# Kernel optimization log

Measured on AMD Instinct MI355X. Metric: run time of the kernel, lower is better.

Reference implementation:

```python
import jax, jax.numpy as jnp
import numpy as np

L = 6          # number of GNN layers
D = 128        # feature_dim (d_model)
H = 4          # num_heads (hardcoded in AttentionalPropagation)
DH = D // H    # per-head dim
N = 2048       # number of segments/keypoints per frame
B = 1          # batch
NAMES = ["self", "cross"] * (L // 2)
EPS = 1e-5     # InstanceNorm1d eps


def _conv1(W, b, x):
    # Conv1d kernel_size=1: W [out,in], x [b,in,n] -> [b,out,n]
    return jnp.einsum('oi,bin->bon', W, x) + b[None, :, None]


def _inorm(x):
    # InstanceNorm1d (affine=False): normalize over the length axis per (batch, channel)
    m = jnp.mean(x, axis=-1, keepdims=True)
    v = jnp.mean((x - m) ** 2, axis=-1, keepdims=True)
    return (x - m) * jax.lax.rsqrt(v + EPS)


def _attn_block(x, src, p):
    Wq, bq, Wk, bk, Wv, bv, Wm, bm, W1, b1, W2, b2 = p
    b_dim, _, n = x.shape
    # view(b, dim, heads, -1): channel axis split as (DH, H)
    q = _conv1(Wq, bq, x).reshape(b_dim, DH, H, -1)
    k = _conv1(Wk, bk, src).reshape(b_dim, DH, H, -1)
    v = _conv1(Wv, bv, src).reshape(b_dim, DH, H, -1)
    scores = jnp.einsum('bdhn,bdhm->bhnm', q, k) / jnp.sqrt(jnp.asarray(DH, x.dtype))
    prob = jax.nn.softmax(scores, axis=-1)
    msg = jnp.einsum('bhnm,bdhm->bdhn', prob, v).reshape(b_dim, D, -1)
    msg = _conv1(Wm, bm, msg)
    # MLP([2D, 2D, D]): Conv1d -> InstanceNorm1d -> ReLU -> Conv1d
    h = _conv1(W1, b1, jnp.concatenate([x, msg], axis=1))
    h = jax.nn.relu(_inorm(h))
    return _conv1(W2, b2, h)


def setup_inputs() -> dict:
    key = jax.random.key(0)
    ks = jax.random.split(key, 14)
    s = 0.05
    f32 = jnp.float32
    return {
        "desc0": jax.random.normal(ks[0], (B, D, N), f32),
        "desc1": jax.random.normal(ks[1], (B, D, N), f32),
        "Wq": jax.random.normal(ks[2], (L, D, D), f32) * s,
        "bq": jnp.zeros((L, D), f32),
        "Wk": jax.random.normal(ks[3], (L, D, D), f32) * s,
        "bk": jnp.zeros((L, D), f32),
        "Wv": jax.random.normal(ks[4], (L, D, D), f32) * s,
        "bv": jnp.zeros((L, D), f32),
        "Wm": jax.random.normal(ks[5], (L, D, D), f32) * s,
        "bm": jnp.zeros((L, D), f32),
        "W1": jax.random.normal(ks[6], (L, 2 * D, 2 * D), f32) * s,
        "b1": jnp.zeros((L, 2 * D), f32),
        "W2": jax.random.normal(ks[7], (L, D, 2 * D), f32) * s,
        "b2": jnp.zeros((L, D), f32),  # nn.init.constant_(mlp[-1].bias, 0.0)
    }


def reference(desc0, desc1, Wq, bq, Wk, bk, Wv, bv, Wm, bm, W1, b1, W2, b2):
    params = (Wq, bq, Wk, bk, Wv, bv, Wm, bm, W1, b1, W2, b2)
    for l in range(L):
        p = tuple(a[l] for a in params)
        if NAMES[l] == 'cross':
            src0, src1 = desc1, desc0
        else:
            src0, src1 = desc0, desc1
        delta0 = _attn_block(desc0, src0, p)
        delta1 = _attn_block(desc1, src1, p)
        desc0 = desc0 + delta0
        desc1 = desc1 + delta1
    return desc0, desc1
```

## Files before the change

### kernel.cpp

```cpp
#include <hip/hip_runtime.h>

#define NN 2048
#define DDIM 128
#define NHEAD 4
#define DH 32
#define NL 6

typedef __attribute__((ext_vector_type(8))) __bf16 bf16x8;
typedef __attribute__((ext_vector_type(4))) float f32x4;

__device__ __forceinline__ unsigned int f2bf(float x) {
  unsigned int u = __float_as_uint(x);
  u += 0x7fff + ((u >> 16) & 1);
  return u >> 16;
}
__device__ __forceinline__ unsigned int pk2(float a, float b) {
  return f2bf(a) | (f2bf(b) << 16);
}
__device__ __forceinline__ float bf2f(unsigned short u) {
  return __uint_as_float(((unsigned int)u) << 16);
}

__global__ __launch_bounds__(256) void wcast_kernel(
    const float* __restrict__ Wq, const float* __restrict__ Wk,
    const float* __restrict__ Wv, const float* __restrict__ W1,
    const float* __restrict__ W2,
    unsigned short* __restrict__ Wqkv, unsigned short* __restrict__ Wb2,
    unsigned short* __restrict__ Wmix) {
  int idx = (blockIdx.x * 256 + threadIdx.x) * 4;
  if (idx >= 688128) return;
  const float* src; unsigned short* dst; int soff, doff;
  if (idx < 98304)       { src = Wq; soff = idx; dst = Wqkv; doff = idx; }
  else if (idx < 196608) { src = Wk; soff = idx - 98304; dst = Wqkv; doff = idx; }
  else if (idx < 294912) { src = Wv; soff = idx - 196608; dst = Wqkv; doff = idx; }
  else if (idx < 491520) { src = W2; soff = idx - 294912; dst = Wb2; doff = soff; }
  else {
    int f = idx - 491520;
    int l = f >> 15, rem = f & 32767;
    int i = rem >> 7, c = rem & 127;
    src = W1; soff = (l << 16) + (i << 8) + c;
    dst = Wmix; doff = (l << 16) + (i << 8) + c;
  }
  float4 v = *(const float4*)&src[soff];
  uint2 p = { pk2(v.x, v.y), pk2(v.z, v.w) };
  *(uint2*)&dst[doff] = p;
}

__global__ __launch_bounds__(256) void wfuse_kernel(
    const float* __restrict__ W1, const float* __restrict__ Wm,
    unsigned short* __restrict__ Wmix,
    const float* __restrict__ bmv, const float* __restrict__ b1,
    float* __restrict__ b1m) {
  const int l = blockIdx.z;
  const int bj = blockIdx.x * 64;
  const int bi = blockIdx.y * 64;
  __shared__ float Ws[32][65];
  __shared__ float Xs[32][64];
  const int t = threadIdx.x;
  const int ti = (t >> 4) << 2;
  const int tj = (t & 15) << 2;
  float acc[4][4] = {{0.f}};
  for (int k0 = 0; k0 < 128; k0 += 32) {
#pragma unroll
    for (int i = 0; i < 8; ++i) {
      int e = t + i * 256;
      int ii = e >> 5, kk = e & 31;
      Ws[kk][ii] = W1[(size_t)(l << 16) + (bi + ii) * 256 + 128 + k0 + kk];
    }
#pragma unroll
    for (int i = 0; i < 2; ++i) {
      int e = t + i * 256;
      int r = e >> 4, c4 = e & 15;
      *(float4*)&Xs[r][c4 * 4] = *(const float4*)&Wm[(size_t)l * 16384 + (k0 + r) * 128 + bj + c4 * 4];
    }
    __syncthreads();
#pragma unroll
    for (int kk = 0; kk < 32; ++kk) {
      float a[4];
      a[0] = Ws[kk][ti]; a[1] = Ws[kk][ti + 1]; a[2] = Ws[kk][ti + 2]; a[3] = Ws[kk][ti + 3];
      float4 b4 = *(const float4*)&Xs[kk][tj];
      float bb[4] = {b4.x, b4.y, b4.z, b4.w};
#pragma unroll
      for (int i = 0; i < 4; ++i)
#pragma unroll
        for (int j = 0; j < 4; ++j) acc[i][j] += a[i] * bb[j];
    }
    __syncthreads();
  }
#pragma unroll
  for (int i = 0; i < 4; ++i) {
    uint2 p = { pk2(acc[i][0], acc[i][1]), pk2(acc[i][2], acc[i][3]) };
    *(uint2*)&Wmix[(size_t)(l << 16) + (bi + ti + i) * 256 + 128 + bj + tj] = p;
  }
  if (blockIdx.x == 0 && blockIdx.y == 0) {
    float a = b1[l * 256 + t];
    const float* wr = &W1[(size_t)(l << 16) + t * 256 + 128];
    const float* bp = &bmv[l * 128];
    for (int k = 0; k < 128; k += 4)
      a += wr[k] * bp[k] + wr[k + 1] * bp[k + 1] + wr[k + 2] * bp[k + 2] + wr[k + 3] * bp[k + 3];
    b1m[l * 256 + t] = a;
  }
}

__global__ __launch_bounds__(256) void desc_cast_kernel(
    const float* __restrict__ d0, const float* __restrict__ d1,
    unsigned short* __restrict__ t0, unsigned short* __restrict__ t1,
    float* __restrict__ o0, float* __restrict__ o1) {
  const float* D = blockIdx.y ? d1 : d0;
  unsigned short* T = blockIdx.y ? t1 : t0;
  float* O = blockIdx.y ? o1 : o0;
  const int n0 = blockIdx.x * 64;
  const int t = threadIdx.x;
  __shared__ __align__(16) unsigned short L[64 * 136];
#pragma unroll
  for (int i = 0; i < 8; ++i) {
    int idx = t + i * 256;
    int c = idx >> 4, nj = (idx & 15) * 4;
    float4 v = *(const float4*)&D[(size_t)c * NN + n0 + nj];
    *(float4*)&O[(size_t)c * NN + n0 + nj] = v;
    L[(nj + 0) * 136 + c] = (unsigned short)f2bf(v.x);
    L[(nj + 1) * 136 + c] = (unsigned short)f2bf(v.y);
    L[(nj + 2) * 136 + c] = (unsigned short)f2bf(v.z);
    L[(nj + 3) * 136 + c] = (unsigned short)f2bf(v.w);
  }
  __syncthreads();
#pragma unroll
  for (int i = 0; i < 4; ++i) {
    int idx = t + i * 256;
    int n = idx >> 4, cj = (idx & 15) * 8;
    uint4 v = *(const uint4*)&L[n * 136 + cj];
    *(uint4*)&T[(size_t)(n0 + n) * 128 + cj] = v;
  }
}

struct MOp {
  const unsigned short* A;
  const float* bias;
  const unsigned short* B1;
  const unsigned short* B2;
  unsigned short* Cb;
  float* Cf;
  const float* Sp;
  int K, ldb, ldc, mode;
};
struct MOps8 { MOp op[8]; };

__global__ __launch_bounds__(256) void mfma_gemm_kernel(MOps8 P) {
  const MOp g = P.op[blockIdx.z];
  const int t = threadIdx.x;
  const int w = t >> 6, lane = t & 63;
  const int col = lane & 15, Qd = lane >> 4;
  const int bm = blockIdx.y * 64;
  const int bn = blockIdx.x * 128;

  __shared__ __align__(16) unsigned short Ws[64 * 40];
  __shared__ __align__(16) unsigned short Xs[128 * 40];
  __shared__ float meanL[256], rstdL[256];
  __shared__ float swS[4][64], swQ[4][64];

  if (g.mode == 4) {
    float s = g.Sp[t * 2], ss = g.Sp[t * 2 + 1];
    float mean = s * (1.0f / NN);
    float var = fmaxf(ss * (1.0f / NN) - mean * mean, 0.f);
    meanL[t] = mean;
    rstdL[t] = rsqrtf(var + 1e-5f);
  }
  if (g.mode == 0 && g.Cf && blockIdx.x == 0 && blockIdx.y == 0) {
    g.Cf[t] = 0.f;
    g.Cf[t + 256] = 0.f;
  }

  f32x4 acc[4][2];
#pragma unroll
  for (int mt = 0; mt < 4; ++mt)
#pragma unroll
    for (int nt = 0; nt < 2; ++nt) acc[mt][nt] = (f32x4){0.f, 0.f, 0.f, 0.f};

  for (int k0 = 0; k0 < g.K; k0 += 32) {
    __syncthreads();
    {
      int row = t >> 2, ko = (t & 3) * 8;
      *(uint4*)&Ws[row * 40 + ko] =
          *(const uint4*)&g.A[(size_t)(bm + row) * g.K + k0 + ko];
    }
    const unsigned short* Bp = g.B1;
    int kk0 = k0;
    if (g.B2 && k0 >= 128) { Bp = g.B2; kk0 = k0 - 128; }
#pragma unroll
    for (int i = 0; i < 2; ++i) {
      int idx = t + i * 256;
      int row = idx >> 2, ko = (idx & 3) * 8;
      uint4 v = *(const uint4*)&Bp[(size_t)(bn + row) * g.ldb + kk0 + ko];
      if (g.mode == 4) {
        union { uint4 q; unsigned short us[8]; } u;
        u.q = v;
#pragma unroll
        for (int j = 0; j < 8; ++j) {
          int k = k0 + ko + j;
          float x = bf2f(u.us[j]);
          x = fmaxf((x - meanL[k]) * rstdL[k], 0.f);
          u.us[j] = (unsigned short)f2bf(x);
        }
        v = u.q;
      }
      *(uint4*)&Xs[row * 40 + ko] = v;
    }
    __syncthreads();
    bf16x8 af[4], bfr[2];
#pragma unroll
    for (int mt = 0; mt < 4; ++mt)
      af[mt] = *(const bf16x8*)&Ws[(mt * 16 + col) * 40 + Qd * 8];
#pragma unroll
    for (int nt = 0; nt < 2; ++nt)
      bfr[nt] = *(const bf16x8*)&Xs[(w * 32 + nt * 16 + col) * 40 + Qd * 8];
#pragma unroll
    for (int mt = 0; mt < 4; ++mt)
#pragma unroll
      for (int nt = 0; nt < 2; ++nt)
        acc[mt][nt] = __builtin_amdgcn_mfma_f32_16x16x32_bf16(af[mt], bfr[nt], acc[mt][nt], 0, 0, 0);
  }

#pragma unroll
  for (int mt = 0; mt < 4; ++mt) {
    const int c0 = bm + mt * 16 + Qd * 4;
    const float b0 = g.bias[c0], b1 = g.bias[c0 + 1];
    const float b2 = g.bias[c0 + 2], b3 = g.bias[c0 + 3];
    float sA[4] = {0.f, 0.f, 0.f, 0.f}, sQ[4] = {0.f, 0.f, 0.f, 0.f};
#pragma unroll
    for (int nt = 0; nt < 2; ++nt) {
      const int n = bn + w * 32 + nt * 16 + col;
      f32x4 a = acc[mt][nt];
      float v0 = a[0] + b0, v1 = a[1] + b1, v2 = a[2] + b2, v3 = a[3] + b3;
      if (g.mode <= 2) {
        if (g.mode == 0) {
          const float sc = 0.25503488f;
          v0 *= sc; v1 *= sc; v2 *= sc; v3 *= sc;
        }
        const int d = c0 >> 2;
        if (g.mode == 1) {
          g.Cb[((size_t)0 * NN + n) * 32 + d] = (unsigned short)f2bf(v0);
          g.Cb[((size_t)1 * NN + n) * 32 + d] = (unsigned short)f2bf(v1);
          g.Cb[((size_t)2 * NN + n) * 32 + d] = (unsigned short)f2bf(v2);
          g.Cb[((size_t)3 * NN + n) * 32 + d] = (unsigned short)f2bf(v3);
        } else {
          g.Cb[(size_t)(0 * 32 + d) * NN + n] = (unsigned short)f2bf(v0);
          g.Cb[(size_t)(1 * 32 + d) * NN + n] = (unsigned short)f2bf(v1);
          g.Cb[(size_t)(2 * 32 + d) * NN + n] = (unsigned short)f2bf(v2);
          g.Cb[(size_t)(3 * 32 + d) * NN + n] = (unsigned short)f2bf(v3);
        }
      } else if (g.mode == 5) {
        uint2 pv = { pk2(v0, v1), pk2(v2, v3) };
        *(uint2*)&g.Cb[(size_t)n * g.ldc + c0] = pv;
        sA[0] += v0; sA[1] += v1; sA[2] += v2; sA[3] += v3;
        sQ[0] += v0 * v0; sQ[1] += v1 * v1; sQ[2] += v2 * v2; sQ[3] += v3 * v3;
      } else {
        float* dp = g.Cf;
        float o0 = dp[(size_t)(c0 + 0) * NN + n] + v0;
        float o1 = dp[(size_t)(c0 + 1) * NN + n] + v1;
        float o2 = dp[(size_t)(c0 + 2) * NN + n] + v2;
        float o3 = dp[(size_t)(c0 + 3) * NN + n] + v3;
        dp[(size_t)(c0 + 0) * NN + n] = o0;
        dp[(size_t)(c0 + 1) * NN + n] = o1;
        dp[(size_t)(c0 + 2) * NN + n] = o2;
        dp[(size_t)(c0 + 3) * NN + n] = o3;
        uint2 pv = { pk2(o0, o1), pk2(o2, o3) };
        *(uint2*)&g.Cb[(size_t)n * 128 + c0] = pv;
      }
    }
    if (g.mode == 5) {
#pragma unroll
      for (int r = 0; r < 4; ++r) {
#pragma unroll
        for (int off = 1; off < 16; off <<= 1) {
          sA[r] += __shfl_xor(sA[r], off);
          sQ[r] += __shfl_xor(sQ[r], off);
        }
      }
      if (col == 0) {
#pragma unroll
        for (int r = 0; r < 4; ++r) {
          swS[w][mt * 16 + Qd * 4 + r] = sA[r];
          swQ[w][mt * 16 + Qd * 4 + r] = sQ[r];
        }
      }
    }
  }
  if (g.mode == 5) {
    __syncthreads();
    if (t < 64) {
      float a = swS[0][t] + swS[1][t] + swS[2][t] + swS[3][t];
      float b = swQ[0][t] + swQ[1][t] + swQ[2][t] + swQ[3][t];
      atomicAdd(&g.Cf[(bm + t) * 2], a);
      atomicAdd(&g.Cf[(bm + t) * 2 + 1], b);
    }
  }
}

__global__ __launch_bounds__(256, 4) void attn_mfma_kernel(
    const unsigned short* __restrict__ Qb0, const unsigned short* __restrict__ Kt0,
    const unsigned short* __restrict__ Vb0, const unsigned short* __restrict__ Qb1,
    const unsigned short* __restrict__ Kt1, const unsigned short* __restrict__ Vb1,
    unsigned short* __restrict__ mgT0, unsigned short* __restrict__ mgT1, int cross) {
  const int z = blockIdx.y, desc = z >> 2, h = z & 3;
  const int t = threadIdx.x;
  const int wid = t >> 6, lane = t & 63;
  const int col = lane & 15, Qd = lane >> 4;
  const int qb = blockIdx.x * 16;

  const unsigned short* Qb = desc ? Qb1 : Qb0;
  const int s = cross ? (1 - desc) : desc;
  const unsigned short* Kt = s ? Kt1 : Kt0;
  const unsigned short* Vb = s ? Vb1 : Vb0;

  __shared__ __align__(16) unsigned short SM[12800];
  unsigned short* KtW = SM + wid * 3200;
  unsigned short* VW = SM + wid * 3200 + 1280;
  unsigned short* PW = SM + wid * 3200 + 2560;

  bf16x8 bq;
  {
    union { unsigned short u[8]; bf16x8 v; } tmp;
#pragma unroll
    for (int j = 0; j < 8; ++j)
      tmp.u[j] = Qb[(size_t)(h * 32 + Qd * 8 + j) * NN + qb + col];
    bq = tmp.v;
  }

  f32x4 o0 = {0.f, 0.f, 0.f, 0.f}, o1 = {0.f, 0.f, 0.f, 0.f};
  float m = -1e30f, l = 0.f;

  const int kq = wid * 512;
  for (int it = 0; it < 16; ++it) {
    const int k0 = kq + it * 32;
#pragma unroll
    for (int jj = 0; jj < 2; ++jj) {
      int e = lane + jj * 64;
      int r4 = e >> 2, seg = (e & 3) * 8;
      *(uint4*)&KtW[r4 * 40 + seg] =
          *(const uint4*)&Kt[((size_t)h * NN + k0 + r4) * 32 + seg];
      *(uint4*)&VW[r4 * 40 + seg] =
          *(const uint4*)&Vb[(size_t)(h * 32 + r4) * NN + k0 + seg];
    }
    bf16x8 aK0 = *(const bf16x8*)&KtW[col * 40 + Qd * 8];
    bf16x8 aK1 = *(const bf16x8*)&KtW[(16 + col) * 40 + Qd * 8];
    bf16x8 av0 = *(const bf16x8*)&VW[col * 40 + Qd * 8];
    bf16x8 av1 = *(const bf16x8*)&VW[(16 + col) * 40 + Qd * 8];
    f32x4 z4 = {0.f, 0.f, 0.f, 0.f};
    f32x4 s0 = __builtin_amdgcn_mfma_f32_16x16x32_bf16(aK0, bq, z4, 0, 0, 0);
    f32x4 s1 = __builtin_amdgcn_mfma_f32_16x16x32_bf16(aK1, bq, z4, 0, 0, 0);
    float cm = fmaxf(fmaxf(fmaxf(s0[0], s0[1]), fmaxf(s0[2], s0[3])),
                     fmaxf(fmaxf(s1[0], s1[1]), fmaxf(s1[2], s1[3])));
    cm = fmaxf(cm, __shfl_xor(cm, 16));
    cm = fmaxf(cm, __shfl_xor(cm, 32));
    const float mn = fmaxf(m, cm);
    const float alpha = exp2f(m - mn);
    m = mn;
    float p00 = exp2f(s0[0] - mn), p01 = exp2f(s0[1] - mn);
    float p02 = exp2f(s0[2] - mn), p03 = exp2f(s0[3] - mn);
    float p10 = exp2f(s1[0] - mn), p11 = exp2f(s1[1] - mn);
    float p12 = exp2f(s1[2] - mn), p13 = exp2f(s1[3] - mn);
    float us = (p00 + p01) + (p02 + p03) + (p10 + p11) + (p12 + p13);
    us += __shfl_xor(us, 16);
    us += __shfl_xor(us, 32);
    l = l * alpha + us;
    uint2 w0 = { pk2(p00, p01), pk2(p02, p03) };
    uint2 w1 = { pk2(p10, p11), pk2(p12, p13) };
    *(uint2*)&PW[col * 40 + Qd * 4] = w0;
    *(uint2*)&PW[col * 40 + 16 + Qd * 4] = w1;
    bf16x8 pb = *(const bf16x8*)&PW[col * 40 + Qd * 8];
    o0 = o0 * alpha;
    o1 = o1 * alpha;
    o0 = __builtin_amdgcn_mfma_f32_16x16x32_bf16(av0, pb, o0, 0, 0, 0);
    o1 = __builtin_amdgcn_mfma_f32_16x16x32_bf16(av1, pb, o1, 0, 0, 0);
  }

  __syncthreads();
  float* fS = (float*)SM;
  *(float4*)&fS[wid * 576 + col * 36 + Qd * 4] =
      make_float4(o0[0], o0[1], o0[2], o0[3]);
  *(float4*)&fS[wid * 576 + col * 36 + 16 + Qd * 4] =
      make_float4(o1[0], o1[1], o1[2], o1[3]);
  if (Qd == 0) {
    fS[2304 + wid * 16 + col] = m;
    fS[2368 + wid * 16 + col] = l;
  }
  __syncthreads();
  {
    const int q16 = t >> 4, dg = t & 15;
    float m0 = fS[2304 + q16], m1 = fS[2304 + 16 + q16];
    float m2 = fS[2304 + 32 + q16], m3 = fS[2304 + 48 + q16];
    float M = fmaxf(fmaxf(m0, m1), fmaxf(m2, m3));
    float w0 = exp2f(m0 - M), w1 = exp2f(m1 - M);
    float w2 = exp2f(m2 - M), w3 = exp2f(m3 - M);
    float L = w0 * fS[2368 + q16] + w1 * fS[2368 + 16 + q16] +
              w2 * fS[2368 + 32 + q16] + w3 * fS[2368 + 48 + q16];
    float inv = 1.0f / L;
    unsigned short* T = desc ? mgT1 : mgT0;
    const int q = qb + q16;
#pragma unroll
    for (int r = 0; r < 2; ++r) {
      int d = dg * 2 + r;
      float v = (w0 * fS[0 * 576 + q16 * 36 + d] + w1 * fS[1 * 576 + q16 * 36 + d] +
                 w2 * fS[2 * 576 + q16 * 36 + d] + w3 * fS[3 * 576 + q16 * 36 + d]) * inv;
      T[(size_t)q * 128 + d * 4 + h] = (unsigned short)f2bf(v);
    }
  }
}

extern "C" void kernel_launch(void* const* d_in, const int* in_sizes, int n_in,
                              void* d_out, int out_size, void* d_ws, size_t ws_size,
                              hipStream_t stream) {
  const float* desc0 = (const float*)d_in[0];
  const float* desc1 = (const float*)d_in[1];
  const float* Wq = (const float*)d_in[2];
  const float* bq = (const float*)d_in[3];
  const float* Wk = (const float*)d_in[4];
  const float* bk = (const float*)d_in[5];
  const float* Wv = (const float*)d_in[6];
  const float* bv = (const float*)d_in[7];
  const float* Wm = (const float*)d_in[8];
  const float* bmv = (const float*)d_in[9];
  const float* W1 = (const float*)d_in[10];
  const float* b1 = (const float*)d_in[11];
  const float* W2 = (const float*)d_in[12];
  const float* b2 = (const float*)d_in[13];

  float* out0 = (float*)d_out;
  float* out1 = out0 + (size_t)DDIM * NN;

  float* fws = (float*)d_ws;
  float* Sg0 = fws;
  float* Sg1 = Sg0 + 512;
  float* b1m = Sg1 + 512;
  unsigned short* uws = (unsigned short*)(b1m + 1536);
  unsigned short* dT0 = uws;
  unsigned short* dT1 = uws + 1 * 262144;
  unsigned short* Qb0 = uws + 2 * 262144;
  unsigned short* Qb1 = uws + 3 * 262144;
  unsigned short* Kt0 = uws + 4 * 262144;
  unsigned short* Kt1 = uws + 5 * 262144;
  unsigned short* Vb0 = uws + 6 * 262144;
  unsigned short* Vb1 = uws + 7 * 262144;
  unsigned short* mgT0 = uws + 8 * 262144;
  unsigned short* mgT1 = uws + 9 * 262144;
  unsigned short* HT0 = uws + 10 * 262144;
  unsigned short* HT1 = HT0 + 524288;
  unsigned short* Wqkv = HT1 + 524288;
  unsigned short* Wb2 = Wqkv + 294912;
  unsigned short* Wmix = Wb2 + 196608;

  wcast_kernel<<<672, 256, 0, stream>>>(Wq, Wk, Wv, W1, W2, Wqkv, Wb2, Wmix);
  wfuse_kernel<<<dim3(2, 4, 6), 256, 0, stream>>>(W1, Wm, Wmix, bmv, b1, b1m);
  desc_cast_kernel<<<dim3(32, 2), 256, 0, stream>>>(desc0, desc1, dT0, dT1, out0, out1);

  for (int l = 0; l < NL; ++l) {
    const int cross = l & 1;
    const unsigned short* wq = Wqkv + l * 16384;
    const unsigned short* wk = Wqkv + 98304 + l * 16384;
    const unsigned short* wv = Wqkv + 196608 + l * 16384;
    const unsigned short* wmx = Wmix + l * 65536;
    const unsigned short* w2 = Wb2 + l * 32768;
    const float* bqp = bq + (size_t)l * 128;
    const float* bkp = bk + (size_t)l * 128;
    const float* bvp = bv + (size_t)l * 128;
    const float* b1p = b1m + (size_t)l * 256;
    const float* b2p = b2 + (size_t)l * 128;

    MOps8 Pq = {};
    Pq.op[0] = {wq, bqp, dT0, nullptr, Qb0, Sg0, nullptr, 128, 128, 0, 0};
    Pq.op[1] = {wq, bqp, dT1, nullptr, Qb1, Sg1, nullptr, 128, 128, 0, 0};
    Pq.op[2] = {wk, bkp, dT0, nullptr, Kt0, nullptr, nullptr, 128, 128, 0, 1};
    Pq.op[3] = {wk, bkp, dT1, nullptr, Kt1, nullptr, nullptr, 128, 128, 0, 1};
    Pq.op[4] = {wv, bvp, dT0, nullptr, Vb0, nullptr, nullptr, 128, 128, 0, 2};
    Pq.op[5] = {wv, bvp, dT1, nullptr, Vb1, nullptr, nullptr, 128, 128, 0, 2};
    mfma_gemm_kernel<<<dim3(16, 2, 6), 256, 0, stream>>>(Pq);

    attn_mfma_kernel<<<dim3(128, 8), 256, 0, stream>>>(
        Qb0, Kt0, Vb0, Qb1, Kt1, Vb1, mgT0, mgT1, cross);

    MOps8 P1 = {};
    P1.op[0] = {wmx, b1p, dT0, mgT0, HT0, Sg0, nullptr, 256, 128, 256, 5};
    P1.op[1] = {wmx, b1p, dT1, mgT1, HT1, Sg1, nullptr, 256, 128, 256, 5};
    mfma_gemm_kernel<<<dim3(16, 4, 2), 256, 0, stream>>>(P1);

    MOps8 P2 = {};
    P2.op[0] = {w2, b2p, HT0, nullptr, dT0, out0, Sg0, 256, 256, 128, 4};
    P2.op[1] = {w2, b2p, HT1, nullptr, dT1, out1, Sg1, 256, 256, 128, 4};
    mfma_gemm_kernel<<<dim3(16, 2, 2), 256, 0, stream>>>(P2);
  }
}
```

Measured before the change: 447.4 us.

## Drop LDS staging in GEMM and attention, merge setup kernels into one launch

```diff
diff --git a/kernel.cpp b/kernel.cpp
--- a/kernel.cpp
+++ b/kernel.cpp
@@ -21,115 +21,115 @@
   return __uint_as_float(((unsigned int)u) << 16);
 }
 
-__global__ __launch_bounds__(256) void wcast_kernel(
+__global__ __launch_bounds__(256) void setup_kernel(
     const float* __restrict__ Wq, const float* __restrict__ Wk,
-    const float* __restrict__ Wv, const float* __restrict__ W1,
-    const float* __restrict__ W2,
+    const float* __restrict__ Wv, const float* __restrict__ Wm,
+    const float* __restrict__ W1, const float* __restrict__ W2,
+    const float* __restrict__ bmv, const float* __restrict__ b1,
+    const float* __restrict__ desc0, const float* __restrict__ desc1,
     unsigned short* __restrict__ Wqkv, unsigned short* __restrict__ Wb2,
-    unsigned short* __restrict__ Wmix) {
-  int idx = (blockIdx.x * 256 + threadIdx.x) * 4;
-  if (idx >= 688128) return;
-  const float* src; unsigned short* dst; int soff, doff;
-  if (idx < 98304)       { src = Wq; soff = idx; dst = Wqkv; doff = idx; }
-  else if (idx < 196608) { src = Wk; soff = idx - 98304; dst = Wqkv; doff = idx; }
-  else if (idx < 294912) { src = Wv; soff = idx - 196608; dst = Wqkv; doff = idx; }
-  else if (idx < 491520) { src = W2; soff = idx - 294912; dst = Wb2; doff = soff; }
-  else {
-    int f = idx - 491520;
-    int l = f >> 15, rem = f & 32767;
-    int i = rem >> 7, c = rem & 127;
-    src = W1; soff = (l << 16) + (i << 8) + c;
-    dst = Wmix; doff = (l << 16) + (i << 8) + c;
-  }
-  float4 v = *(const float4*)&src[soff];
-  uint2 p = { pk2(v.x, v.y), pk2(v.z, v.w) };
-  *(uint2*)&dst[doff] = p;
-}
-
-__global__ __launch_bounds__(256) void wfuse_kernel(
-    const float* __restrict__ W1, const float* __restrict__ Wm,
-    unsigned short* __restrict__ Wmix,
-    const float* __restrict__ bmv, const float* __restrict__ b1,
-    float* __restrict__ b1m) {
-  const int l = blockIdx.z;
-  const int bj = blockIdx.x * 64;
-  const int bi = blockIdx.y * 64;
-  __shared__ float Ws[32][65];
-  __shared__ float Xs[32][64];
+    unsigned short* __restrict__ Wmix, float* __restrict__ b1m,
+    unsigned short* __restrict__ dT0, unsigned short* __restrict__ dT1,
+    float* __restrict__ o0, float* __restrict__ o1) {
+  __shared__ __align__(16) unsigned char ARENA[17408];
+  const int bid = blockIdx.x;
   const int t = threadIdx.x;
-  const int ti = (t >> 4) << 2;
-  const int tj = (t & 15) << 2;
-  float acc[4][4] = {{0.f}};
-  for (int k0 = 0; k0 < 128; k0 += 32) {
+
+  if (bid < 672) {
+    int idx = (bid * 256 + t) * 4;
+    if (idx >= 688128) return;
+    const float* src; unsigned short* dst; int soff, doff;
+    if (idx < 98304)       { src = Wq; soff = idx; dst = Wqkv; doff = idx; }
+    else if (idx < 196608) { src = Wk; soff = idx - 98304; dst = Wqkv; doff = idx; }
+    else if (idx < 294912) { src = Wv; soff = idx - 196608; dst = Wqkv; doff = idx; }
+    else if (idx < 491520) { src = W2; soff = idx - 294912; dst = Wb2; doff = soff; }
+    else {
+      int f = idx - 491520;
+      int l = f >> 15, rem = f & 32767;
+      int i = rem >> 7, c = rem & 127;
+      src = W1; soff = (l << 16) + (i << 8) + c;
+      dst = Wmix; doff = (l << 16) + (i << 8) + c;
+    }
+    float4 v = *(const float4*)&src[soff];
+    uint2 p = { pk2(v.x, v.y), pk2(v.z, v.w) };
+    *(uint2*)&dst[doff] = p;
+  } else if (bid < 720) {
+    const int b = bid - 672;
+    const int jb = b & 1, ib = (b >> 1) & 3, l = b >> 3;
+    const int bj = jb * 64, bi = ib * 64;
+    float* Ws = (float*)ARENA;
+    float* Xs = (float*)ARENA + 2080;
+    const int ti = (t >> 4) << 2;
+    const int tj = (t & 15) << 2;
+    float acc[4][4] = {{0.f}};
+    for (int k0 = 0; k0 < 128; k0 += 32) {
+#pragma unroll
+      for (int i = 0; i < 8; ++i) {
+        int e = t + i * 256;
+        int ii = e >> 5, kk = e & 31;
+        Ws[kk * 65 + ii] = W1[(size_t)(l << 16) + (bi + ii) * 256 + 128 + k0 + kk];
+      }
+#pragma unroll
+      for (int i = 0; i < 2; ++i) {
+        int e = t + i * 256;
+        int r = e >> 4, c4 = e & 15;
+        *(float4*)&Xs[r * 64 + c4 * 4] =
+            *(const float4*)&Wm[(size_t)l * 16384 + (k0 + r) * 128 + bj + c4 * 4];
+      }
+      __syncthreads();
+#pragma unroll
+      for (int kk = 0; kk < 32; ++kk) {
+        float a[4];
+        a[0] = Ws[kk * 65 + ti]; a[1] = Ws[kk * 65 + ti + 1];
+        a[2] = Ws[kk * 65 + ti + 2]; a[3] = Ws[kk * 65 + ti + 3];
+        float4 b4 = *(const float4*)&Xs[kk * 64 + tj];
+        float bb[4] = {b4.x, b4.y, b4.z, b4.w};
+#pragma unroll
+        for (int i = 0; i < 4; ++i)
+#pragma unroll
+          for (int j = 0; j < 4; ++j) acc[i][j] += a[i] * bb[j];
+      }
+      __syncthreads();
+    }
+#pragma unroll
+    for (int i = 0; i < 4; ++i) {
+      uint2 p = { pk2(acc[i][0], acc[i][1]), pk2(acc[i][2], acc[i][3]) };
+      *(uint2*)&Wmix[(size_t)(l << 16) + (bi + ti + i) * 256 + 128 + bj + tj] = p;
+    }
+    if (jb == 0 && ib == 0) {
+      float a = b1[l * 256 + t];
+      const float* wr = &W1[(size_t)(l << 16) + t * 256 + 128];
+      const float* bp = &bmv[l * 128];
+      for (int k = 0; k < 128; k += 4)
+        a += wr[k] * bp[k] + wr[k + 1] * bp[k + 1] + wr[k + 2] * bp[k + 2] + wr[k + 3] * bp[k + 3];
+      b1m[l * 256 + t] = a;
+    }
+  } else {
+    const int b = bid - 720;
+    const float* D = (b >> 5) ? desc1 : desc0;
+    unsigned short* T = (b >> 5) ? dT1 : dT0;
+    float* O = (b >> 5) ? o1 : o0;
+    const int n0 = (b & 31) * 64;
+    unsigned short* L = (unsigned short*)ARENA;
 #pragma unroll
     for (int i = 0; i < 8; ++i) {
-      int e = t + i * 256;
-      int ii = e >> 5, kk = e & 31;
-      Ws[kk][ii] = W1[(size_t)(l << 16) + (bi + ii) * 256 + 128 + k0 + kk];
-    }
-#pragma unroll
-    for (int i = 0; i < 2; ++i) {
-      int e = t + i * 256;
-      int r = e >> 4, c4 = e & 15;
-      *(float4*)&Xs[r][c4 * 4] = *(const float4*)&Wm[(size_t)l * 16384 + (k0 + r) * 128 + bj + c4 * 4];
+      int idx = t + i * 256;
+      int c = idx >> 4, nj = (idx & 15) * 4;
+      float4 v = *(const float4*)&D[(size_t)c * NN + n0 + nj];
+      *(float4*)&O[(size_t)c * NN + n0 + nj] = v;
+      L[(nj + 0) * 136 + c] = (unsigned short)f2bf(v.x);
+      L[(nj + 1) * 136 + c] = (unsigned short)f2bf(v.y);
+      L[(nj + 2) * 136 + c] = (unsigned short)f2bf(v.z);
+      L[(nj + 3) * 136 + c] = (unsigned short)f2bf(v.w);
     }
     __syncthreads();
 #pragma unroll
-    for (int kk = 0; kk < 32; ++kk) {
-      float a[4];
-      a[0] = Ws[kk][ti]; a[1] = Ws[kk][ti + 1]; a[2] = Ws[kk][ti + 2]; a[3] = Ws[kk][ti + 3];
-      float4 b4 = *(const float4*)&Xs[kk][tj];
-      float bb[4] = {b4.x, b4.y, b4.z, b4.w};
-#pragma unroll
-      for (int i = 0; i < 4; ++i)
-#pragma unroll
-        for (int j = 0; j < 4; ++j) acc[i][j] += a[i] * bb[j];
-    }
-    __syncthreads();
-  }
-#pragma unroll
-  for (int i = 0; i < 4; ++i) {
-    uint2 p = { pk2(acc[i][0], acc[i][1]), pk2(acc[i][2], acc[i][3]) };
-    *(uint2*)&Wmix[(size_t)(l << 16) + (bi + ti + i) * 256 + 128 + bj + tj] = p;
-  }
-  if (blockIdx.x == 0 && blockIdx.y == 0) {
-    float a = b1[l * 256 + t];
-    const float* wr = &W1[(size_t)(l << 16) + t * 256 + 128];
-    const float* bp = &bmv[l * 128];
-    for (int k = 0; k < 128; k += 4)
-      a += wr[k] * bp[k] + wr[k + 1] * bp[k + 1] + wr[k + 2] * bp[k + 2] + wr[k + 3] * bp[k + 3];
-    b1m[l * 256 + t] = a;
-  }
-}
-
-__global__ __launch_bounds__(256) void desc_cast_kernel(
-    const float* __restrict__ d0, const float* __restrict__ d1,
-    unsigned short* __restrict__ t0, unsigned short* __restrict__ t1,
-    float* __restrict__ o0, float* __restrict__ o1) {
-  const float* D = blockIdx.y ? d1 : d0;
-  unsigned short* T = blockIdx.y ? t1 : t0;
-  float* O = blockIdx.y ? o1 : o0;
-  const int n0 = blockIdx.x * 64;
-  const int t = threadIdx.x;
-  __shared__ __align__(16) unsigned short L[64 * 136];
-#pragma unroll
-  for (int i = 0; i < 8; ++i) {
-    int idx = t + i * 256;
-    int c = idx >> 4, nj = (idx & 15) * 4;
-    float4 v = *(const float4*)&D[(size_t)c * NN + n0 + nj];
-    *(float4*)&O[(size_t)c * NN + n0 + nj] = v;
-    L[(nj + 0) * 136 + c] = (unsigned short)f2bf(v.x);
-    L[(nj + 1) * 136 + c] = (unsigned short)f2bf(v.y);
-    L[(nj + 2) * 136 + c] = (unsigned short)f2bf(v.z);
-    L[(nj + 3) * 136 + c] = (unsigned short)f2bf(v.w);
-  }
-  __syncthreads();
-#pragma unroll
-  for (int i = 0; i < 4; ++i) {
-    int idx = t + i * 256;
-    int n = idx >> 4, cj = (idx & 15) * 8;
-    uint4 v = *(const uint4*)&L[n * 136 + cj];
-    *(uint4*)&T[(size_t)(n0 + n) * 128 + cj] = v;
+    for (int i = 0; i < 4; ++i) {
+      int idx = t + i * 256;
+      int n = idx >> 4, cj = (idx & 15) * 8;
+      uint4 v = *(const uint4*)&L[n * 136 + cj];
+      *(uint4*)&T[(size_t)(n0 + n) * 128 + cj] = v;
+    }
   }
 }
 
@@ -141,20 +141,19 @@
   unsigned short* Cb;
   float* Cf;
   const float* Sp;
-  int K, ldb, ldc, mode;
+  int ldb, ldc, mode;
 };
 struct MOps8 { MOp op[8]; };
 
-__global__ __launch_bounds__(256) void mfma_gemm_kernel(MOps8 P) {
+template <int K>
+__global__ __launch_bounds__(256) void gemm_direct_kernel(MOps8 P) {
   const MOp g = P.op[blockIdx.z];
   const int t = threadIdx.x;
   const int w = t >> 6, lane = t & 63;
   const int col = lane & 15, Qd = lane >> 4;
   const int bm = blockIdx.y * 64;
-  const int bn = blockIdx.x * 128;
-
-  __shared__ __align__(16) unsigned short Ws[64 * 40];
-  __shared__ __align__(16) unsigned short Xs[128 * 40];
+  const int bn = blockIdx.x * 64;
+
   __shared__ float meanL[256], rstdL[256];
   __shared__ float swS[4][64], swQ[4][64];
 
@@ -169,55 +168,47 @@
     g.Cf[t] = 0.f;
     g.Cf[t + 256] = 0.f;
   }
-
-  f32x4 acc[4][2];
-#pragma unroll
-  for (int mt = 0; mt < 4; ++mt)
-#pragma unroll
-    for (int nt = 0; nt < 2; ++nt) acc[mt][nt] = (f32x4){0.f, 0.f, 0.f, 0.f};
-
-  for (int k0 = 0; k0 < g.K; k0 += 32) {
-    __syncthreads();
-    {
-      int row = t >> 2, ko = (t & 3) * 8;
-      *(uint4*)&Ws[row * 40 + ko] =
-          *(const uint4*)&g.A[(size_t)(bm + row) * g.K + k0 + ko];
-    }
+  __syncthreads();
+
+  const int n = bn + w * 16 + col;
+  f32x4 acc[4];
+#pragma unroll
+  for (int mt = 0; mt < 4; ++mt) acc[mt] = (f32x4){0.f, 0.f, 0.f, 0.f};
+
+#pragma unroll
+  for (int k0 = 0; k0 < K; k0 += 32) {
+    bf16x8 af[4];
+#pragma unroll
+    for (int mt = 0; mt < 4; ++mt)
+      af[mt] = *(const bf16x8*)&g.A[(size_t)(bm + mt * 16 + col) * K + k0 + Qd * 8];
     const unsigned short* Bp = g.B1;
-    int kk0 = k0;
-    if (g.B2 && k0 >= 128) { Bp = g.B2; kk0 = k0 - 128; }
-#pragma unroll
-    for (int i = 0; i < 2; ++i) {
-      int idx = t + i * 256;
-      int row = idx >> 2, ko = (idx & 3) * 8;
-      uint4 v = *(const uint4*)&Bp[(size_t)(bn + row) * g.ldb + kk0 + ko];
-      if (g.mode == 4) {
-        union { uint4 q; unsigned short us[8]; } u;
-        u.q = v;
-#pragma unroll
-        for (int j = 0; j < 8; ++j) {
-          int k = k0 + ko + j;
-          float x = bf2f(u.us[j]);
-          x = fmaxf((x - meanL[k]) * rstdL[k], 0.f);
-          u.us[j] = (unsigned short)f2bf(x);
-        }
-        v = u.q;
-      }
-      *(uint4*)&Xs[row * 40 + ko] = v;
-    }
-    __syncthreads();
-    bf16x8 af[4], bfr[2];
+    int kk = k0;
+    if (g.B2 && k0 >= 128) { Bp = g.B2; kk = k0 - 128; }
+    uint4 v = *(const uint4*)&Bp[(size_t)n * g.ldb + kk + Qd * 8];
+    if (g.mode == 4) {
+      float4 mA = *(const float4*)&meanL[k0 + Qd * 8];
+      float4 mB = *(const float4*)&meanL[k0 + Qd * 8 + 4];
+      float4 rA = *(const float4*)&rstdL[k0 + Qd * 8];
+      float4 rB = *(const float4*)&rstdL[k0 + Qd * 8 + 4];
+      union { uint4 q; unsigned short us[8]; } u;
+      u.q = v;
+      float x0 = fmaxf((bf2f(u.us[0]) - mA.x) * rA.x, 0.f);
+      float x1 = fmaxf((bf2f(u.us[1]) - mA.y) * rA.y, 0.f);
+      float x2 = fmaxf((bf2f(u.us[2]) - mA.z) * rA.z, 0.f);
+      float x3 = fmaxf((bf2f(u.us[3]) - mA.w) * rA.w, 0.f);
+      float x4 = fmaxf((bf2f(u.us[4]) - mB.x) * rB.x, 0.f);
+      float x5 = fmaxf((bf2f(u.us[5]) - mB.y) * rB.y, 0.f);
+      float x6 = fmaxf((bf2f(u.us[6]) - mB.z) * rB.z, 0.f);
+      float x7 = fmaxf((bf2f(u.us[7]) - mB.w) * rB.w, 0.f);
+      u.q.x = pk2(x0, x1); u.q.y = pk2(x2, x3);
+      u.q.z = pk2(x4, x5); u.q.w = pk2(x6, x7);
+      v = u.q;
+    }
+    union { uint4 q; bf16x8 b; } bc;
+    bc.q = v;
 #pragma unroll
     for (int mt = 0; mt < 4; ++mt)
-      af[mt] = *(const bf16x8*)&Ws[(mt * 16 + col) * 40 + Qd * 8];
-#pragma unroll
-    for (int nt = 0; nt < 2; ++nt)
-      bfr[nt] = *(const bf16x8*)&Xs[(w * 32 + nt * 16 + col) * 40 + Qd * 8];
-#pragma unroll
-    for (int mt = 0; mt < 4; ++mt)
-#pragma unroll
-      for (int nt = 0; nt < 2; ++nt)
-        acc[mt][nt] = __builtin_amdgcn_mfma_f32_16x16x32_bf16(af[mt], bfr[nt], acc[mt][nt], 0, 0, 0);
+      acc[mt] = __builtin_amdgcn_mfma_f32_16x16x32_bf16(af[mt], bc.b, acc[mt], 0, 0, 0);
   }
 
 #pragma unroll
@@ -225,49 +216,30 @@
     const int c0 = bm + mt * 16 + Qd * 4;
     const float b0 = g.bias[c0], b1 = g.bias[c0 + 1];
     const float b2 = g.bias[c0 + 2], b3 = g.bias[c0 + 3];
-    float sA[4] = {0.f, 0.f, 0.f, 0.f}, sQ[4] = {0.f, 0.f, 0.f, 0.f};
-#pragma unroll
-    for (int nt = 0; nt < 2; ++nt) {
-      const int n = bn + w * 32 + nt * 16 + col;
-      f32x4 a = acc[mt][nt];
-      float v0 = a[0] + b0, v1 = a[1] + b1, v2 = a[2] + b2, v3 = a[3] + b3;
-      if (g.mode <= 2) {
-        if (g.mode == 0) {
-          const float sc = 0.25503488f;
-          v0 *= sc; v1 *= sc; v2 *= sc; v3 *= sc;
-        }
-        const int d = c0 >> 2;
-        if (g.mode == 1) {
-          g.Cb[((size_t)0 * NN + n) * 32 + d] = (unsigned short)f2bf(v0);
-          g.Cb[((size_t)1 * NN + n) * 32 + d] = (unsigned short)f2bf(v1);
-          g.Cb[((size_t)2 * NN + n) * 32 + d] = (unsigned short)f2bf(v2);
-          g.Cb[((size_t)3 * NN + n) * 32 + d] = (unsigned short)f2bf(v3);
-        } else {
-          g.Cb[(size_t)(0 * 32 + d) * NN + n] = (unsigned short)f2bf(v0);
-          g.Cb[(size_t)(1 * 32 + d) * NN + n] = (unsigned short)f2bf(v1);
-          g.Cb[(size_t)(2 * 32 + d) * NN + n] = (unsigned short)f2bf(v2);
-          g.Cb[(size_t)(3 * 32 + d) * NN + n] = (unsigned short)f2bf(v3);
-        }
-      } else if (g.mode == 5) {
-        uint2 pv = { pk2(v0, v1), pk2(v2, v3) };
-        *(uint2*)&g.Cb[(size_t)n * g.ldc + c0] = pv;
-        sA[0] += v0; sA[1] += v1; sA[2] += v2; sA[3] += v3;
-        sQ[0] += v0 * v0; sQ[1] += v1 * v1; sQ[2] += v2 * v2; sQ[3] += v3 * v3;
+    f32x4 a = acc[mt];
+    float v0 = a[0] + b0, v1 = a[1] + b1, v2 = a[2] + b2, v3 = a[3] + b3;
+    if (g.mode <= 2) {
+      if (g.mode == 0) {
+        const float sc = 0.25503488f;
+        v0 *= sc; v1 *= sc; v2 *= sc; v3 *= sc;
+      }
+      const int d = c0 >> 2;
+      if (g.mode == 1) {
+        g.Cb[((size_t)0 * NN + n) * 32 + d] = (unsigned short)f2bf(v0);
+        g.Cb[((size_t)1 * NN + n) * 32 + d] = (unsigned short)f2bf(v1);
+        g.Cb[((size_t)2 * NN + n) * 32 + d] = (unsigned short)f2bf(v2);
+        g.Cb[((size_t)3 * NN + n) * 32 + d] = (unsigned short)f2bf(v3);
       } else {
-        float* dp = g.Cf;
-        float o0 = dp[(size_t)(c0 + 0) * NN + n] + v0;
-        float o1 = dp[(size_t)(c0 + 1) * NN + n] + v1;
-        float o2 = dp[(size_t)(c0 + 2) * NN + n] + v2;
-        float o3 = dp[(size_t)(c0 + 3) * NN + n] + v3;
-        dp[(size_t)(c0 + 0) * NN + n] = o0;
-        dp[(size_t)(c0 + 1) * NN + n] = o1;
-        dp[(size_t)(c0 + 2) * NN + n] = o2;
-        dp[(size_t)(c0 + 3) * NN + n] = o3;
-        uint2 pv = { pk2(o0, o1), pk2(o2, o3) };
-        *(uint2*)&g.Cb[(size_t)n * 128 + c0] = pv;
-      }
-    }
-    if (g.mode == 5) {
+        g.Cb[(size_t)(0 * 32 + d) * NN + n] = (unsigned short)f2bf(v0);
+        g.Cb[(size_t)(1 * 32 + d) * NN + n] = (unsigned short)f2bf(v1);
+        g.Cb[(size_t)(2 * 32 + d) * NN + n] = (unsigned short)f2bf(v2);
+        g.Cb[(size_t)(3 * 32 + d) * NN + n] = (unsigned short)f2bf(v3);
+      }
+    } else if (g.mode == 5) {
+      uint2 pv = { pk2(v0, v1), pk2(v2, v3) };
+      *(uint2*)&g.Cb[(size_t)n * g.ldc + c0] = pv;
+      float sA[4] = {v0, v1, v2, v3};
+      float sQ[4] = {v0 * v0, v1 * v1, v2 * v2, v3 * v3};
 #pragma unroll
       for (int r = 0; r < 4; ++r) {
 #pragma unroll
@@ -283,6 +255,18 @@
           swQ[w][mt * 16 + Qd * 4 + r] = sQ[r];
         }
       }
+    } else {
+      float* dp = g.Cf;
+      float o0 = dp[(size_t)(c0 + 0) * NN + n] + v0;
+      float o1 = dp[(size_t)(c0 + 1) * NN + n] + v1;
+      float o2 = dp[(size_t)(c0 + 2) * NN + n] + v2;
+      float o3 = dp[(size_t)(c0 + 3) * NN + n] + v3;
+      dp[(size_t)(c0 + 0) * NN + n] = o0;
+      dp[(size_t)(c0 + 1) * NN + n] = o1;
+      dp[(size_t)(c0 + 2) * NN + n] = o2;
+      dp[(size_t)(c0 + 3) * NN + n] = o3;
+      uint2 pv = { pk2(o0, o1), pk2(o2, o3) };
+      *(uint2*)&g.Cb[(size_t)n * g.ldc + c0] = pv;
     }
   }
   if (g.mode == 5) {
@@ -312,10 +296,9 @@
   const unsigned short* Kt = s ? Kt1 : Kt0;
   const unsigned short* Vb = s ? Vb1 : Vb0;
 
-  __shared__ __align__(16) unsigned short SM[12800];
-  unsigned short* KtW = SM + wid * 3200;
-  unsigned short* VW = SM + wid * 3200 + 1280;
-  unsigned short* PW = SM + wid * 3200 + 2560;
+  __shared__ __align__(16) unsigned short SM[7424];
+  unsigned short* PW = SM + wid * 640;
+  float* fS = (float*)(SM + 2560);
 
   bf16x8 bq;
   {
@@ -330,21 +313,13 @@
   float m = -1e30f, l = 0.f;
 
   const int kq = wid * 512;
+#pragma unroll 2
   for (int it = 0; it < 16; ++it) {
     const int k0 = kq + it * 32;
-#pragma unroll
-    for (int jj = 0; jj < 2; ++jj) {
-      int e = lane + jj * 64;
-      int r4 = e >> 2, seg = (e & 3) * 8;
-      *(uint4*)&KtW[r4 * 40 + seg] =
-          *(const uint4*)&Kt[((size_t)h * NN + k0 + r4) * 32 + seg];
-      *(uint4*)&VW[r4 * 40 + seg] =
-          *(const uint4*)&Vb[(size_t)(h * 32 + r4) * NN + k0 + seg];
-    }
-    bf16x8 aK0 = *(const bf16x8*)&KtW[col * 40 + Qd * 8];
-    bf16x8 aK1 = *(const bf16x8*)&KtW[(16 + col) * 40 + Qd * 8];
-    bf16x8 av0 = *(const bf16x8*)&VW[col * 40 + Qd * 8];
-    bf16x8 av1 = *(const bf16x8*)&VW[(16 + col) * 40 + Qd * 8];
+    bf16x8 aK0 = *(const bf16x8*)&Kt[((size_t)h * NN + k0 + col) * 32 + Qd * 8];
+    bf16x8 aK1 = *(const bf16x8*)&Kt[((size_t)h * NN + k0 + 16 + col) * 32 + Qd * 8];
+    bf16x8 av0 = *(const bf16x8*)&Vb[(size_t)(h * 32 + col) * NN + k0 + Qd * 8];
+    bf16x8 av1 = *(const bf16x8*)&Vb[(size_t)(h * 32 + 16 + col) * NN + k0 + Qd * 8];
     f32x4 z4 = {0.f, 0.f, 0.f, 0.f};
     f32x4 s0 = __builtin_amdgcn_mfma_f32_16x16x32_bf16(aK0, bq, z4, 0, 0, 0);
     f32x4 s1 = __builtin_amdgcn_mfma_f32_16x16x32_bf16(aK1, bq, z4, 0, 0, 0);
@@ -375,7 +350,6 @@
   }
 
   __syncthreads();
-  float* fS = (float*)SM;
   *(float4*)&fS[wid * 576 + col * 36 + Qd * 4] =
       make_float4(o0[0], o0[1], o0[2], o0[3]);
   *(float4*)&fS[wid * 576 + col * 36 + 16 + Qd * 4] =
@@ -449,9 +423,9 @@
   unsigned short* Wb2 = Wqkv + 294912;
   unsigned short* Wmix = Wb2 + 196608;
 
-  wcast_kernel<<<672, 256, 0, stream>>>(Wq, Wk, Wv, W1, W2, Wqkv, Wb2, Wmix);
-  wfuse_kernel<<<dim3(2, 4, 6), 256, 0, stream>>>(W1, Wm, Wmix, bmv, b1, b1m);
-  desc_cast_kernel<<<dim3(32, 2), 256, 0, stream>>>(desc0, desc1, dT0, dT1, out0, out1);
+  setup_kernel<<<784, 256, 0, stream>>>(Wq, Wk, Wv, Wm, W1, W2, bmv, b1,
+                                        desc0, desc1, Wqkv, Wb2, Wmix, b1m,
+                                        dT0, dT1, out0, out1);
 
   for (int l = 0; l < NL; ++l) {
     const int cross = l & 1;
@@ -467,25 +441,25 @@
     const float* b2p = b2 + (size_t)l * 128;
 
     MOps8 Pq = {};
-    Pq.op[0] = {wq, bqp, dT0, nullptr, Qb0, Sg0, nullptr, 128, 128, 0, 0};
-    Pq.op[1] = {wq, bqp, dT1, nullptr, Qb1, Sg1, nullptr, 128, 128, 0, 0};
-    Pq.op[2] = {wk, bkp, dT0, nullptr, Kt0, nullptr, nullptr, 128, 128, 0, 1};
-    Pq.op[3] = {wk, bkp, dT1, nullptr, Kt1, nullptr, nullptr, 128, 128, 0, 1};
-    Pq.op[4] = {wv, bvp, dT0, nullptr, Vb0, nullptr, nullptr, 128, 128, 0, 2};
-    Pq.op[5] = {wv, bvp, dT1, nullptr, Vb1, nullptr, nullptr, 128, 128, 0, 2};
-    mfma_gemm_kernel<<<dim3(16, 2, 6), 256, 0, stream>>>(Pq);
+    Pq.op[0] = {wq, bqp, dT0, nullptr, Qb0, Sg0, nullptr, 128, 0, 0};
+    Pq.op[1] = {wq, bqp, dT1, nullptr, Qb1, Sg1, nullptr, 128, 0, 0};
+    Pq.op[2] = {wk, bkp, dT0, nullptr, Kt0, nullptr, nullptr, 128, 0, 1};
+    Pq.op[3] = {wk, bkp, dT1, nullptr, Kt1, nullptr, nullptr, 128, 0, 1};
+    Pq.op[4] = {wv, bvp, dT0, nullptr, Vb0, nullptr, nullptr, 128, 0, 2};
+    Pq.op[5] = {wv, bvp, dT1, nullptr, Vb1, nullptr, nullptr, 128, 0, 2};
+    gemm_direct_kernel<128><<<dim3(32, 2, 6), 256, 0, stream>>>(Pq);
 
     attn_mfma_kernel<<<dim3(128, 8), 256, 0, stream>>>(
         Qb0, Kt0, Vb0, Qb1, Kt1, Vb1, mgT0, mgT1, cross);
 
     MOps8 P1 = {};
-    P1.op[0] = {wmx, b1p, dT0, mgT0, HT0, Sg0, nullptr, 256, 128, 256, 5};
-    P1.op[1] = {wmx, b1p, dT1, mgT1, HT1, Sg1, nullptr, 256, 128, 256, 5};
-    mfma_gemm_kernel<<<dim3(16, 4, 2), 256, 0, stream>>>(P1);
+    P1.op[0] = {wmx, b1p, dT0, mgT0, HT0, Sg0, nullptr, 128, 256, 5};
+    P1.op[1] = {wmx, b1p, dT1, mgT1, HT1, Sg1, nullptr, 128, 256, 5};
+    gemm_direct_kernel<256><<<dim3(32, 4, 2), 256, 0, stream>>>(P1);
 
     MOps8 P2 = {};
-    P2.op[0] = {w2, b2p, HT0, nullptr, dT0, out0, Sg0, 256, 256, 128, 4};
-    P2.op[1] = {w2, b2p, HT1, nullptr, dT1, out1, Sg1, 256, 256, 128, 4};
-    mfma_gemm_kernel<<<dim3(16, 2, 2), 256, 0, stream>>>(P2);
-  }
-}
+    P2.op[0] = {w2, b2p, HT0, nullptr, dT0, out0, Sg0, 256, 128, 4};
+    P2.op[1] = {w2, b2p, HT1, nullptr, dT1, out1, Sg1, 256, 128, 4};
+    gemm_direct_kernel<256><<<dim3(32, 2, 2), 256, 0, stream>>>(P2);
+  }
+}
```

Result: faster. 425.0 us (-5.0%).
